# Kernel tuning notes

Measured on AMD Instinct MI355X. Metric: run time of the kernel, lower is better.

Reference implementation:

```python
import jax, jax.numpy as jnp
import numpy as np

NUM_HEADS = 32
NUM_KV_HEADS = 8
HEAD_DIM = 128
ROPE_THETA = 10000.0


def rotate_half(x):
    half = x.shape[-1] // 2
    return jnp.concatenate((-x[..., half:], x[..., :half]), axis=-1)


def setup_inputs() -> dict:
    key = jax.random.key(0)
    k1, k2, k3 = jax.random.split(key, 3)
    B, S, H = 2, 2048, 4096
    qkv_out = (NUM_KV_HEADS * 2 + NUM_HEADS) * HEAD_DIM  # 6144
    hidden_states = jax.random.normal(k1, (B, S, H), dtype=jnp.float32)
    position_ids = jnp.broadcast_to(jnp.arange(S, dtype=jnp.int64 if jax.config.jax_enable_x64 else jnp.int32)[None, :], (B, S))
    w_qkv = jax.random.normal(k2, (qkv_out, H), dtype=jnp.float32) * (1.0 / np.sqrt(H))
    w_dense = jax.random.normal(k3, (H, H), dtype=jnp.float32) * (1.0 / np.sqrt(H))
    return {"hidden_states": hidden_states, "position_ids": position_ids, "w_qkv": w_qkv, "w_dense": w_dense}


def reference(hidden_states, position_ids, w_qkv, w_dense):
    B, S, H = hidden_states.shape
    nh, nkv, hd = NUM_HEADS, NUM_KV_HEADS, HEAD_DIM
    g = nh // nkv  # query heads per kv head

    # fused QKV projection (FalconLinear, no bias)
    fused = hidden_states @ w_qkv.T  # [B, S, (nkv*(g+2))*hd]

    # new_decoder_architecture split: [B, S, nkv, g+2, hd]
    qkv = fused.reshape(B, S, nkv, g + 2, hd)
    q = qkv[:, :, :, :-2]                 # [B, S, nkv, g, hd]
    k = qkv[:, :, :, -2:-1]               # [B, S, nkv, 1, hd]
    v = qkv[:, :, :, -1:]
    k = jnp.broadcast_to(k, q.shape)      # GQA broadcast to all query heads
    v = jnp.broadcast_to(v, q.shape)
    # flatten kv-head/group dims -> [B, S, nh, hd], then [B, nh, S, hd]
    q = q.reshape(B, S, nh, hd).transpose(0, 2, 1, 3)
    k = k.reshape(B, S, nh, hd).transpose(0, 2, 1, 3)
    v = v.reshape(B, S, nh, hd).transpose(0, 2, 1, 3)

    # default RoPE (attention_scaling = 1.0)
    inv_freq = 1.0 / (ROPE_THETA ** (jnp.arange(0, hd, 2, dtype=jnp.float32) / hd))  # [hd/2]
    freqs = position_ids.astype(jnp.float32)[:, :, None] * inv_freq[None, None, :]   # [B, S, hd/2]
    emb = jnp.concatenate((freqs, freqs), axis=-1)                                    # [B, S, hd]
    cos = jnp.cos(emb)[:, None].astype(hidden_states.dtype)                           # [B, 1, S, hd]
    sin = jnp.sin(emb)[:, None].astype(hidden_states.dtype)
    q = q * cos + rotate_half(q) * sin
    k = k * cos + rotate_half(k) * sin

    # causal SDPA
    scale = 1.0 / np.sqrt(hd)
    scores = jnp.einsum('bhqd,bhkd->bhqk', q, k) * scale  # [B, nh, S, S]
    causal = jnp.tril(jnp.ones((S, S), dtype=bool))
    scores = jnp.where(causal[None, None], scores, jnp.finfo(scores.dtype).min)
    attn = jax.nn.softmax(scores, axis=-1)
    ctx = jnp.einsum('bhqk,bhkd->bhqd', attn, v)          # [B, nh, S, hd]

    # merge heads + output dense
    ctx = ctx.transpose(0, 2, 1, 3).reshape(B, S, nh * hd)
    return ctx @ w_dense.T
```

## Files before the change

### kernel.cpp

```cpp
#include <hip/hip_runtime.h>

typedef __bf16 bf16_t;
typedef __bf16 bf16x8 __attribute__((ext_vector_type(8)));
typedef __bf16 bf16x4 __attribute__((ext_vector_type(4)));
typedef __bf16 bf16x2 __attribute__((ext_vector_type(2)));
typedef float  f32x4  __attribute__((ext_vector_type(4)));
typedef float  f32x16 __attribute__((ext_vector_type(16)));
typedef unsigned int u32x4 __attribute__((ext_vector_type(4)));

#define MFMA16(a, b, c) __builtin_amdgcn_mfma_f32_16x16x32_bf16((a), (b), (c), 0, 0, 0)
#define MFMA32(a, b, c) __builtin_amdgcn_mfma_f32_32x32x16_bf16((a), (b), (c), 0, 0, 0)

__device__ __forceinline__ void async_load16(const void* g, void* l) {
    __builtin_amdgcn_global_load_lds(
        (const __attribute__((address_space(1))) void*)g,
        (__attribute__((address_space(3))) void*)l, 16, 0, 0);
}

__device__ __forceinline__ unsigned pack2(float a, float b) {
    bf16x2 t;
    t[0] = (bf16_t)a;
    t[1] = (bf16_t)b;
    return __builtin_bit_cast(unsigned, t);
}

__global__ void cvt3_f32_to_bf16(const float* __restrict__ s0, bf16_t* __restrict__ d0, int n0,
                                 const float* __restrict__ s1, bf16_t* __restrict__ d1, int n1,
                                 const float* __restrict__ s2, bf16_t* __restrict__ d2, int n2) {
    const float* s; bf16_t* d; int n, bl, nb;
    const int bid = blockIdx.x;
    if (bid < 512)       { s = s0; d = d0; n = n0; bl = bid;        nb = 512; }
    else if (bid < 1280) { s = s1; d = d1; n = n1; bl = bid - 512;  nb = 768; }
    else                 { s = s2; d = d2; n = n2; bl = bid - 1280; nb = 512; }
    const int stride4 = nb * blockDim.x * 4;
    for (int j = (bl * blockDim.x + threadIdx.x) * 4; j < n; j += stride4) {
        float4 v = *(const float4*)(s + j);
        bf16x4 o = { (bf16_t)v.x, (bf16_t)v.y, (bf16_t)v.z, (bf16_t)v.w };
        *(bf16x4*)(d + j) = o;
    }
}

__device__ __forceinline__ void storeC(float* C, size_t idx, float v)  { C[idx] = v; }
__device__ __forceinline__ void storeC(bf16_t* C, size_t idx, float v) { C[idx] = (bf16_t)v; }

template <typename OT>
__global__ __launch_bounds__(512, 2) void gemm256(const bf16_t* __restrict__ A,
                                                  const bf16_t* __restrict__ B,
                                                  OT* __restrict__ C,
                                                  int M, int N, int K) {
    __shared__ __align__(16) bf16_t lds[2][2][2][128][64];
    const int tid  = threadIdx.x;
    const int lane = tid & 63;
    const int wid  = tid >> 6;
    const int lrow = lane & 15, lhi = lane >> 4;
    const int wrow = (wid >> 2) * 64;
    const int wcol = (wid & 3) * 32;
    const int NT = K >> 6;
    const int nbx = N >> 8;

    const int nwg = gridDim.x;
    const int w = ((int)blockIdx.x & 7) * (nwg >> 3) + ((int)blockIdx.x >> 3);
    const size_t m0 = (size_t)(w / nbx) * 256;
    const size_t n0 = (size_t)(w % nbx) * 256;

    const int cmask = ((lrow & 1) << 5) | ((lrow & 2) << 3) | ((lrow & 4) << 1);
    const int cK0 = (lhi * 8) ^ cmask;
    const int cK1 = (32 + lhi * 8) ^ cmask;
    const int r8 = lane >> 3;
    const int gcol = ((lane & 7) * 8) ^ (((r8 & 1) << 5) | ((r8 & 2) << 3) | ((r8 & 4) << 1));

    auto stage = [&](const bf16_t* srcBase, bf16_t* region) {
#pragma unroll
        for (int c = 0; c < 2; ++c)
            async_load16(srcBase + (size_t)(c * 64 + wid * 8 + r8) * K + gcol,
                         region + c * 4096 + wid * 512);
    };

    int buf = 0;
    bf16x8 af[2][4];
    bf16x8 b0f[2][2], b1f[2][2];

    auto loadA = [&](int mh) {
#pragma unroll
        for (int i = 0; i < 4; ++i) {
            const bf16_t* rp = &lds[buf][0][mh][wrow + i * 16 + lrow][0];
            af[0][i] = *(const bf16x8*)(rp + cK0);
            af[1][i] = *(const bf16x8*)(rp + cK1);
        }
    };
    auto loadB = [&](int nh, bf16x8 (&bf)[2][2]) {
#pragma unroll
        for (int j = 0; j < 2; ++j) {
            const bf16_t* rp = &lds[buf][1][nh][wcol + j * 16 + lrow][0];
            bf[0][j] = *(const bf16x8*)(rp + cK0);
            bf[1][j] = *(const bf16x8*)(rp + cK1);
        }
    };
    auto mmacc = [&](f32x4 (&acc)[4][2], bf16x8 (&bf)[2][2]) {
#pragma unroll
        for (int kk = 0; kk < 2; ++kk)
#pragma unroll
            for (int i = 0; i < 4; ++i)
#pragma unroll
                for (int j = 0; j < 2; ++j)
                    acc[i][j] = MFMA16(af[kk][i], bf[kk][j], acc[i][j]);
    };

    f32x4 a00[4][2], a01[4][2], a10[4][2], a11[4][2];
    const f32x4 vz = {0.f, 0.f, 0.f, 0.f};
#pragma unroll
    for (int i = 0; i < 4; ++i)
#pragma unroll
        for (int j = 0; j < 2; ++j) { a00[i][j] = vz; a01[i][j] = vz; a10[i][j] = vz; a11[i][j] = vz; }

    const bf16_t* Am = A + m0 * K;
    const bf16_t* Bn = B + n0 * K;

    stage(Am,                     &lds[0][0][0][0][0]);
    stage(Bn,                     &lds[0][1][0][0][0]);
    stage(Bn + (size_t)128 * K,   &lds[0][1][1][0][0]);
    stage(Am + (size_t)128 * K,   &lds[0][0][1][0][0]);
    stage(Am + 64,                &lds[1][0][0][0][0]);
    stage(Bn + 64,                &lds[1][1][0][0][0]);
    asm volatile("s_waitcnt vmcnt(4)" ::: "memory");
    __builtin_amdgcn_s_barrier();

    for (int u = 0; u < NT; ++u, buf ^= 1) {
        loadA(0);
        loadB(0, b0f);
        loadB(1, b1f);
        __builtin_amdgcn_s_barrier();
        asm volatile("s_waitcnt lgkmcnt(0)" ::: "memory");
        if (u + 1 < NT) {
            stage(Bn + (size_t)(u + 1) * 64 + (size_t)128 * K, &lds[buf ^ 1][1][1][0][0]);
            stage(Am + (size_t)(u + 1) * 64 + (size_t)128 * K, &lds[buf ^ 1][0][1][0][0]);
        }
        __builtin_amdgcn_s_setprio(1);
        mmacc(a00, b0f);
        mmacc(a01, b1f);
        __builtin_amdgcn_s_setprio(0);
        __builtin_amdgcn_s_barrier();
        loadA(1);
        __builtin_amdgcn_s_barrier();
        asm volatile("s_waitcnt lgkmcnt(0)" ::: "memory");
        if (u + 2 < NT) {
            stage(Am + (size_t)(u + 2) * 64, &lds[buf][0][0][0][0]);
            stage(Bn + (size_t)(u + 2) * 64, &lds[buf][1][0][0][0]);
        }
        __builtin_amdgcn_s_setprio(1);
        mmacc(a10, b0f);
        mmacc(a11, b1f);
        __builtin_amdgcn_s_setprio(0);
        if (u == NT - 2)     asm volatile("s_waitcnt vmcnt(0)" ::: "memory");
        else if (u < NT - 2) asm volatile("s_waitcnt vmcnt(4)" ::: "memory");
        __builtin_amdgcn_s_barrier();
    }

    auto storeQ = [&](f32x4 (&acc)[4][2], int mq, int nq) {
#pragma unroll
        for (int i = 0; i < 4; ++i)
#pragma unroll
            for (int j = 0; j < 2; ++j)
#pragma unroll
                for (int r = 0; r < 4; ++r) {
                    size_t row = m0 + mq * 128 + wrow + i * 16 + lhi * 4 + r;
                    size_t col = n0 + nq * 128 + wcol + j * 16 + lrow;
                    storeC(C, row * (size_t)N + col, acc[i][j][r]);
                }
    };
    storeQ(a00, 0, 0); storeQ(a01, 0, 1); storeQ(a10, 1, 0); storeQ(a11, 1, 1);
}

__global__ void rope_scatter(const bf16_t* __restrict__ fused, const int* __restrict__ pos_ids,
                             bf16_t* __restrict__ Q, bf16_t* __restrict__ Kb) {
    const int token = blockIdx.x;
    const int b = token >> 11, s = token & 2047;
    const int d = threadIdx.x;
    const float pos = (float)pos_ids[token];
    const float inv = __expf(-(float)d * (9.210340371976184f / 64.0f));
    float sn, c;
    sincosf(pos * inv, &sn, &c);
    const bf16_t* frow = fused + (size_t)token * 6144;
    for (int it = 0; it < 5; ++it) {
        int ss = it * 8 + threadIdx.y;
        int col;
        bf16_t* outp;
        if (ss < 32) {
            int h = ss, kv = h >> 2, gi = h & 3;
            col  = kv * 768 + gi * 128 + d;
            outp = Q + (((size_t)b * 32 + h) * 2048 + s) * 128 + d;
        } else {
            int kv = ss - 32;
            col  = kv * 768 + 512 + d;
            outp = Kb + (((size_t)b * 8 + kv) * 2048 + s) * 128 + d;
        }
        float x0 = (float)frow[col];
        float x1 = (float)frow[col + 64];
        outp[0]  = (bf16_t)(x0 * c - x1 * sn);
        outp[64] = (bf16_t)(x1 * c + x0 * sn);
    }
}

__global__ void v_transpose(const bf16_t* __restrict__ fused, bf16_t* __restrict__ Vt) {
    __shared__ bf16_t tile[32][33];
    const int s0 = blockIdx.x * 32;
    const int d0 = blockIdx.y * 32;
    const int bk = blockIdx.z;
    const int b = bk >> 3, kv = bk & 7;
    const int col0 = kv * 768 + 640 + d0;
    const int tx = threadIdx.x, ty = threadIdx.y;
#pragma unroll
    for (int i = 0; i < 4; i++) {
        int sy = ty + i * 8;
        tile[sy][tx] = fused[((size_t)b * 2048 + s0 + sy) * 6144 + col0 + tx];
    }
    __syncthreads();
#pragma unroll
    for (int i = 0; i < 4; i++) {
        int dy = ty + i * 8;
        Vt[((size_t)bk * 128 + d0 + dy) * 2048 + s0 + tx] = tile[tx][dy];
    }
}

__global__ __launch_bounds__(256) void attn_fwd6(const bf16_t* __restrict__ Q,
                                                 const bf16_t* __restrict__ Kb,
                                                 const bf16_t* __restrict__ Vt,
                                                 bf16_t* __restrict__ ctx) {
    __shared__ __align__(16) bf16_t Ks[2][32][128];
    __shared__ __align__(16) bf16_t Vs[2][128][32];
    const int tid  = threadIdx.x;
    const int lane = tid & 63;
    const int wid  = tid >> 6;
    const int l31  = lane & 31;
    const int hi   = lane >> 5;

    const int bidx  = blockIdx.x;
    const int slot  = bidx >> 8;
    const int rr    = (bidx >> 4) & 15;
    const int combo = bidx & 15;
    const int b     = combo & 1;
    const int kvh   = combo >> 1;
    int qt;
    switch (slot) {
        case 0: qt = rr;      break;
        case 1: qt = 63 - rr; break;
        case 2: qt = 16 + rr; break;
        default: qt = 47 - rr; break;
    }
    const int q0 = qt * 32;
    const int h  = kvh * 4 + wid;

    const bf16_t* kbase = Kb + (((size_t)b * 8 + kvh) * 2048) * 128;
    const bf16_t* vbase = Vt + (((size_t)b * 8 + kvh) * 128) * 2048;
    const float kl = 0.12750062133361622f;

    auto stageKV = [&](int bufi, int kv0) {
#pragma unroll
        for (int c = 0; c < 2; ++c) {
            int q = tid + 256 * c;
            int r = q >> 4;
            int cl = ((q & 15) * 16) ^ ((r & 7) << 4);
            async_load16(kbase + (size_t)(kv0 + r) * 128 + (cl >> 1),
                         &Ks[bufi][0][0] + q * 8);
        }
#pragma unroll
        for (int c = 0; c < 2; ++c) {
            int q = tid + 256 * c;
            int d = q >> 2;
            int cl = ((q & 3) * 16) ^ ((d & 3) << 4);
            async_load16(vbase + (size_t)d * 2048 + kv0 + (cl >> 1),
                         &Vs[bufi][0][0] + q * 8);
        }
    };

    const bf16_t* qbase = Q + (((size_t)b * 32 + h) * 2048 + q0) * 128;
    bf16x8 qf[8];
#pragma unroll
    for (int kc = 0; kc < 8; ++kc)
        qf[kc] = *(const bf16x8*)(qbase + (size_t)l31 * 128 + kc * 16 + hi * 8);

    f32x16 o[4];
#pragma unroll
    for (int db = 0; db < 4; ++db)
#pragma unroll
        for (int r = 0; r < 16; ++r) o[db][r] = 0.f;
    float m = -1e30f, lsum = 0.f;

    const int kxor = (l31 & 7) << 3;
    const int vxor = (l31 & 3) << 3;

    stageKV(0, 0);
    __syncthreads();

    int buf = 0;
    for (int st = 0; st <= qt; ++st, buf ^= 1) {
        if (st < qt) stageKV(buf ^ 1, (st + 1) * 32);

        const bf16_t* krow = &Ks[buf][l31][0];
        f32x16 s;
#pragma unroll
        for (int r = 0; r < 16; ++r) s[r] = 0.f;
#pragma unroll
        for (int kc = 0; kc < 8; kc += 2) {
            bf16x8 k0 = *(const bf16x8*)(krow + ((kc * 16 + hi * 8) ^ kxor));
            bf16x8 k1 = *(const bf16x8*)(krow + (((kc + 1) * 16 + hi * 8) ^ kxor));
            s = MFMA32(k0, qf[kc], s);
            s = MFMA32(k1, qf[kc + 1], s);
        }

        if (st == qt) {
            const int qg = q0 + l31;
            const int kv0 = st * 32;
#pragma unroll
            for (int r = 0; r < 16; ++r) {
                int kvg = kv0 + (r & 3) + 8 * (r >> 2) + 4 * hi;
                if (kvg > qg) s[r] = -1e30f;
            }
        }
        float mx01 = fmaxf(s[0], s[1]);
#pragma unroll
        for (int r = 2; r < 16; r += 2) mx01 = fmaxf(mx01, fmaxf(s[r], s[r + 1]));
        float pmax = fmaxf(mx01, __shfl_xor(mx01, 32, 64));
        if (pmax > m + 90.5f) {
            float corr = exp2f((m - pmax) * kl);
            lsum *= corr;
#pragma unroll
            for (int db = 0; db < 4; ++db)
#pragma unroll
                for (int r = 0; r < 16; ++r) o[db][r] *= corr;
            m = pmax;
        }
        const float mk = m * kl;
        float ps4[4] = {0.f, 0.f, 0.f, 0.f};
#pragma unroll
        for (int r = 0; r < 16; ++r) {
            float e = exp2f(fmaf(s[r], kl, -mk));
            s[r] = e;
            ps4[r & 3] += e;
        }
        lsum += (ps4[0] + ps4[1]) + (ps4[2] + ps4[3]);

#pragma unroll
        for (int ks = 0; ks < 2; ++ks) {
            unsigned u0 = pack2(s[ks * 8 + 0], s[ks * 8 + 1]);
            unsigned u1 = pack2(s[ks * 8 + 2], s[ks * 8 + 3]);
            unsigned u2 = pack2(s[ks * 8 + 4], s[ks * 8 + 5]);
            unsigned u3 = pack2(s[ks * 8 + 6], s[ks * 8 + 7]);
            unsigned t0 = __shfl_xor(u0, 32, 64);
            unsigned t1 = __shfl_xor(u1, 32, 64);
            unsigned t2 = __shfl_xor(u2, 32, 64);
            unsigned t3 = __shfl_xor(u3, 32, 64);
            u32x4 uw;
            uw[0] = hi ? t2 : u0;
            uw[1] = hi ? t3 : u1;
            uw[2] = hi ? u2 : t0;
            uw[3] = hi ? u3 : t1;
            bf16x8 pb = __builtin_bit_cast(bf16x8, uw);
            const int vcol = (ks * 16 + hi * 8) ^ vxor;
#pragma unroll
            for (int db = 0; db < 4; ++db) {
                bf16x8 vf = *(const bf16x8*)(&Vs[buf][db * 32 + l31][0] + vcol);
                o[db] = MFMA32(vf, pb, o[db]);
            }
        }
        __syncthreads();
    }

    float lall = lsum + __shfl_xor(lsum, 32, 64);
    const float inv = 1.0f / lall;
    bf16_t* cb = ctx + ((size_t)(b * 2048 + q0 + l31)) * 4096 + h * 128;
#pragma unroll
    for (int db = 0; db < 4; ++db)
#pragma unroll
        for (int g = 0; g < 4; ++g) {
            bf16x4 w;
#pragma unroll
            for (int i = 0; i < 4; ++i) w[i] = (bf16_t)(o[db][g * 4 + i] * inv);
            *(bf16x4*)(cb + db * 32 + g * 8 + hi * 4) = w;
        }
}

extern "C" void kernel_launch(void* const* d_in, const int* in_sizes, int n_in,
                              void* d_out, int out_size, void* d_ws, size_t ws_size,
                              hipStream_t stream) {
    const float* hs   = (const float*)d_in[0];
    const int*   pos  = (const int*)d_in[1];
    const float* wqkv = (const float*)d_in[2];
    const float* wd   = (const float*)d_in[3];
    float* out = (float*)d_out;
    char* ws = (char*)d_ws;

    bf16_t* Xb    = (bf16_t*)(ws + 0ull);
    bf16_t* Wqkvb = (bf16_t*)(ws + 33554432ull);
    bf16_t* Wdb   = (bf16_t*)(ws + 83886080ull);
    bf16_t* fused = (bf16_t*)(ws + 117440512ull);
    bf16_t* Kb    = (bf16_t*)(ws + 167772160ull);
    bf16_t* Vt    = (bf16_t*)(ws + 176160768ull);
    bf16_t* Qb    = Xb;
    bf16_t* ctx   = fused;

    cvt3_f32_to_bf16<<<1792, 256, 0, stream>>>(hs, Xb, 16777216,
                                               wqkv, Wqkvb, 25165824,
                                               wd, Wdb, 16777216);

    gemm256<bf16_t><<<384, 512, 0, stream>>>(Xb, Wqkvb, fused, 4096, 6144, 4096);

    rope_scatter<<<4096, dim3(64, 8), 0, stream>>>(fused, pos, Qb, Kb);
    v_transpose<<<dim3(64, 4, 16), dim3(32, 8), 0, stream>>>(fused, Vt);

    attn_fwd6<<<1024, 256, 0, stream>>>(Qb, Kb, Vt, ctx);

    gemm256<float><<<256, 512, 0, stream>>>(ctx, Wdb, out, 4096, 4096, 4096);
}
```

Baseline: 592.4 us.

## Add dedicated QKV GEMM with 256x384 tiles processed in two halves

Replaces the generic 256x256 GEMM for the QKV projection with a specialized kernel where each block owns a 256x384 output tile, computed as two 192-column halves. The grid drops from 384 to 256 blocks, so on a 256-CU part it runs as one wave instead of leaving a partial second wave. The cost is that the A tile is reloaded for each half, and the 256x192 tile per pass has a different per-wave MFMA shape and register footprint.

```diff
diff --git a/kernel.cpp b/kernel.cpp
--- a/kernel.cpp
+++ b/kernel.cpp
@@ -42,6 +42,109 @@
 
 __device__ __forceinline__ void storeC(float* C, size_t idx, float v)  { C[idx] = v; }
 __device__ __forceinline__ void storeC(bf16_t* C, size_t idx, float v) { C[idx] = (bf16_t)v; }
+
+__global__ __launch_bounds__(512, 2) void gemm_qkv(const bf16_t* __restrict__ A,
+                                                   const bf16_t* __restrict__ B,
+                                                   bf16_t* __restrict__ C,
+                                                   int M, int N, int K) {
+    __shared__ __align__(16) bf16_t ldsA[2][256][64];
+    __shared__ __align__(16) bf16_t ldsB[2][192][64];
+    const int tid  = threadIdx.x;
+    const int lane = tid & 63;
+    const int wid  = tid >> 6;
+    const int lrow = lane & 15, lhi = lane >> 4;
+    const int wrow = (wid >> 1) * 64;
+    const int wcol = (wid & 1) * 96;
+    const int NT = K >> 6;
+
+    const int nwg = gridDim.x;
+    const int w = ((int)blockIdx.x & 7) * (nwg >> 3) + ((int)blockIdx.x >> 3);
+    const int nbx = N / 384;
+    const size_t m0 = (size_t)(w / nbx) * 256;
+    const size_t n0b = (size_t)(w % nbx) * 384;
+
+    const int cm = (((lrow & 1) << 5) | ((lrow & 2) << 3) | ((lrow & 4) << 1));
+
+    const bf16_t* Am = A + m0 * K;
+
+    auto stageA = [&](int bufi, int k0) {
+#pragma unroll
+        for (int c = 0; c < 4; ++c) {
+            int q = tid + 512 * c;
+            int row = q >> 3, slot = q & 7;
+            int gc = (slot * 8) ^ (((row & 1) << 5) | ((row & 2) << 3) | ((row & 4) << 1));
+            async_load16(Am + (size_t)row * K + k0 + gc, &ldsA[bufi][0][0] + q * 8);
+        }
+    };
+    auto stageB = [&](const bf16_t* Bn, int bufi, int k0) {
+#pragma unroll
+        for (int c = 0; c < 3; ++c) {
+            int q = tid + 512 * c;
+            int row = q >> 3, slot = q & 7;
+            int gc = (slot * 8) ^ (((row & 1) << 5) | ((row & 2) << 3) | ((row & 4) << 1));
+            async_load16(Bn + (size_t)row * K + k0 + gc, &ldsB[bufi][0][0] + q * 8);
+        }
+    };
+
+    for (int half = 0; half < 2; ++half) {
+        const bf16_t* Bn = B + (n0b + half * 192) * K;
+
+        f32x4 acc[4][6];
+        const f32x4 vz = {0.f, 0.f, 0.f, 0.f};
+#pragma unroll
+        for (int i = 0; i < 4; ++i)
+#pragma unroll
+            for (int j = 0; j < 6; ++j) acc[i][j] = vz;
+
+        stageA(0, 0);
+        stageB(Bn, 0, 0);
+        stageA(1, 64);
+        stageB(Bn, 1, 64);
+        asm volatile("s_waitcnt vmcnt(7)" ::: "memory");
+        __builtin_amdgcn_s_barrier();
+
+        for (int u = 0; u < NT; ++u) {
+            const int cur = u & 1;
+            __builtin_amdgcn_s_setprio(1);
+#pragma unroll
+            for (int kk = 0; kk < 2; ++kk) {
+                const int cb = kk * 32 + lhi * 8;
+                bf16x8 af[4], bfv[6];
+#pragma unroll
+                for (int i = 0; i < 4; ++i)
+                    af[i] = *(const bf16x8*)(&ldsA[cur][wrow + i * 16 + lrow][0] + (cb ^ cm));
+#pragma unroll
+                for (int j = 0; j < 6; ++j)
+                    bfv[j] = *(const bf16x8*)(&ldsB[cur][wcol + j * 16 + lrow][0] + (cb ^ cm));
+#pragma unroll
+                for (int i = 0; i < 4; ++i)
+#pragma unroll
+                    for (int j = 0; j < 6; ++j)
+                        acc[i][j] = MFMA16(af[i], bfv[j], acc[i][j]);
+            }
+            __builtin_amdgcn_s_setprio(0);
+            __builtin_amdgcn_s_barrier();
+            if (u + 2 < NT) {
+                stageA(cur, (u + 2) * 64);
+                stageB(Bn, cur, (u + 2) * 64);
+            }
+            if (u == NT - 2)     asm volatile("s_waitcnt vmcnt(0)" ::: "memory");
+            else if (u < NT - 2) asm volatile("s_waitcnt vmcnt(7)" ::: "memory");
+            __builtin_amdgcn_s_barrier();
+        }
+
+#pragma unroll
+        for (int i = 0; i < 4; ++i)
+#pragma unroll
+            for (int j = 0; j < 6; ++j)
+#pragma unroll
+                for (int r = 0; r < 4; ++r) {
+                    size_t row = m0 + wrow + i * 16 + lhi * 4 + r;
+                    size_t col = n0b + half * 192 + wcol + j * 16 + lrow;
+                    C[row * (size_t)N + col] = (bf16_t)acc[i][j][r];
+                }
+    }
+}
 
 template <typename OT>
 __global__ __launch_bounds__(512, 2) void gemm256(const bf16_t* __restrict__ A,
@@ -403,7 +506,7 @@
                                                wqkv, Wqkvb, 25165824,
                                                wd, Wdb, 16777216);
 
-    gemm256<bf16_t><<<384, 512, 0, stream>>>(Xb, Wqkvb, fused, 4096, 6144, 4096);
+    gemm_qkv<<<256, 512, 0, stream>>>(Xb, Wqkvb, fused, 4096, 6144, 4096);
 
     rope_scatter<<<4096, dim3(64, 8), 0, stream>>>(fused, pos, Qb, Kb);
     v_transpose<<<dim3(64, 4, 16), dim3(32, 8), 0, stream>>>(fused, Vt);
```

After: 572.3 us. 3.4% less time.
